# Kernel tuning notes

Measured on AMD Instinct MI355X. Metric: run time of the kernel, lower is better.

The kernel has to match this reference:

```python
import jax, jax.numpy as jnp
import numpy as np

EPS = 1e-5


def setup_inputs() -> dict:
    key = jax.random.key(0)
    ks = jax.random.split(key, 12)
    N, E, H, NIN = 50000, 800000, 128, 256  # nodes, edges, num_hidden, num_in
    D_IN = H + NIN  # 384, concat width
    src_na = jax.random.normal(ks[0], (N, H), dtype=jnp.float32)
    dst_na = jax.random.normal(ks[1], (N, H), dtype=jnp.float32)
    ea = jax.random.normal(ks[2], (E, H), dtype=jnp.float32)
    edge_idx = jax.random.randint(ks[3], (2, E), 0, N, dtype=jnp.int64)
    s = 0.05
    W11 = jax.random.normal(ks[4], (D_IN, H), dtype=jnp.float32) * s
    b11 = jnp.zeros((H,), dtype=jnp.float32)
    W12 = jax.random.normal(ks[5], (H, H), dtype=jnp.float32) * s
    b12 = jnp.zeros((H,), dtype=jnp.float32)
    W13 = jax.random.normal(ks[6], (H, H), dtype=jnp.float32) * s
    b13 = jnp.zeros((H,), dtype=jnp.float32)
    gamma = jnp.ones((H,), dtype=jnp.float32)
    beta = jnp.zeros((H,), dtype=jnp.float32)
    return {"src_na": src_na, "dst_na": dst_na, "ea": ea, "edge_idx": edge_idx,
            "W11": W11, "b11": b11, "W12": W12, "b12": b12,
            "W13": W13, "b13": b13, "gamma": gamma, "beta": beta}


def reference(src_na, dst_na, ea, edge_idx, W11, b11, W12, b12, W13, b13, gamma, beta):
    dst_idx = edge_idx[0]
    src_idx = edge_idx[1]
    # gather endpoint node features per edge, concat: [E, H + 2*H_node]
    h_EV = jnp.concatenate([src_na[src_idx], ea, dst_na[dst_idx]], axis=-1)
    gelu = lambda x: jax.nn.gelu(x, approximate=False)  # torch GELU is exact erf
    h = gelu(h_EV @ W11 + b11)
    h = gelu(h @ W12 + b12)
    h_message = h @ W13 + b13
    # dropout in eval mode = identity; BatchNorm1d with batch stats (training-style)
    x = ea + h_message
    mean = jnp.mean(x, axis=0)
    var = jnp.var(x, axis=0)  # biased, as BatchNorm uses for normalization
    ea_update = (x - mean) * jax.lax.rsqrt(var + EPS) * gamma + beta
    return ea_update
```

## Files before the change

kernel.cpp:

```cpp
#include <hip/hip_runtime.h>
#include <hip/hip_fp16.h>

#define HD 128
#define BM 128

typedef _Float16 f16x8 __attribute__((ext_vector_type(8)));
typedef float f32x4 __attribute__((ext_vector_type(4)));

#define W11H_OFF 0
#define W11L_OFF 49152
#define W12H_OFF 98304
#define W12L_OFF 114688
#define W13H_OFF 131072
#define W13L_OFF 147456

__device__ __forceinline__ float gelu_exact(float x) {
  return 0.5f * x * (1.0f + erff(x * 0.70710678118654752f));
}

__global__ __launch_bounds__(256) void repack_w(
    const float* __restrict__ W11, const float* __restrict__ W12,
    const float* __restrict__ W13, _Float16* __restrict__ wp)
{
  int t = blockIdx.x * 256 + threadIdx.x;
  const float* W; int local, hb, lb;
  if (t < 6144)      { W = W11; local = t;        hb = W11H_OFF; lb = W11L_OFF; }
  else if (t < 8192) { W = W12; local = t - 6144; hb = W12H_OFF; lb = W12L_OFF; }
  else               { W = W13; local = t - 8192; hb = W13H_OFF; lb = W13L_OFF; }
  int frag = local >> 6, lane = local & 63;
  int k0  = (frag >> 3) * 32 + ((lane >> 4) * 8);
  int col = (frag & 7) * 16 + (lane & 15);
  _Float16* Hp = wp + hb + (size_t)local * 8;
  _Float16* Lp = wp + lb + (size_t)local * 8;
#pragma unroll
  for (int i = 0; i < 8; ++i) {
    float w = W[(size_t)(k0 + i) * HD + col];
    _Float16 h = (_Float16)w;
    Hp[i] = h;
    Lp[i] = (_Float16)(w - (float)h);
  }
}

__global__ __launch_bounds__(256, 2) void fused_mlp(
    const float* __restrict__ src_na, const float* __restrict__ dst_na,
    const float* __restrict__ ea, const int* __restrict__ eidx,
    const float* __restrict__ b11, const float* __restrict__ b12,
    const float* __restrict__ b13, const _Float16* __restrict__ wp,
    float* __restrict__ stats, float* __restrict__ xout, int E)
{
  __shared__ unsigned int hsm[4 * 32 * HD];
  const int tid  = threadIdx.x;
  const int lane = tid & 63;
  const int wave = tid >> 6;
  const int l15  = lane & 15;
  const int lg   = lane >> 4;
  const int e0   = blockIdx.x * BM + wave * 32;
  unsigned int* myh = hsm + wave * 32 * HD;

  int erow[2], sidx[2], didx[2];
#pragma unroll
  for (int m = 0; m < 2; ++m) {
    int e = e0 + m * 16 + l15;
    e = e < E ? e : E - 1;
    erow[m] = e;
    didx[m] = eidx[e];
    sidx[m] = eidx[E + e];
  }

  const f32x4 vzero = {0.f, 0.f, 0.f, 0.f};
  f32x4 acc[2][8];
#pragma unroll
  for (int m = 0; m < 2; ++m)
#pragma unroll
    for (int f = 0; f < 8; ++f) acc[m][f] = vzero;

  const _Float16* w11h = wp + W11H_OFF;
  const _Float16* w11l = wp + W11L_OFF;
#pragma unroll 2
  for (int ks = 0; ks < 12; ++ks) {
    const int part = ks >> 2;
    const int kc = (ks & 3) * 32 + lg * 8;
    f16x8 ah[2], al[2];
#pragma unroll
    for (int m = 0; m < 2; ++m) {
      const float* rp;
      if (part == 0)      rp = src_na + (size_t)sidx[m] * HD;
      else if (part == 1) rp = ea + (size_t)erow[m] * HD;
      else                rp = dst_na + (size_t)didx[m] * HD;
      float4 v0 = *(const float4*)(rp + kc);
      float4 v1 = *(const float4*)(rp + kc + 4);
      float v[8] = {v0.x, v0.y, v0.z, v0.w, v1.x, v1.y, v1.z, v1.w};
#pragma unroll
      for (int i = 0; i < 8; ++i) {
        _Float16 hh = (_Float16)v[i];
        ah[m][i] = hh;
        al[m][i] = (_Float16)(v[i] - (float)hh);
      }
    }
    const _Float16* bhp = w11h + (size_t)(ks * 8) * 512 + lane * 8;
    const _Float16* blp = w11l + (size_t)(ks * 8) * 512 + lane * 8;
#pragma unroll
    for (int fc = 0; fc < 8; ++fc) {
      f16x8 bh = *(const f16x8*)(bhp + fc * 512);
      f16x8 bl = *(const f16x8*)(blp + fc * 512);
#pragma unroll
      for (int m = 0; m < 2; ++m) {
        acc[m][fc] = __builtin_amdgcn_mfma_f32_16x16x32_f16(ah[m], bh, acc[m][fc], 0, 0, 0);
        acc[m][fc] = __builtin_amdgcn_mfma_f32_16x16x32_f16(ah[m], bl, acc[m][fc], 0, 0, 0);
        acc[m][fc] = __builtin_amdgcn_mfma_f32_16x16x32_f16(al[m], bh, acc[m][fc], 0, 0, 0);
      }
    }
  }

  auto store_h = [&](const float* __restrict__ bias) {
#pragma unroll
    for (int fc = 0; fc < 8; ++fc) {
      int col = fc * 16 + l15;
      float b = bias[col];
#pragma unroll
      for (int m = 0; m < 2; ++m)
#pragma unroll
        for (int r = 0; r < 4; ++r) {
          int row = m * 16 + lg * 4 + r;
          float hv = gelu_exact(acc[m][fc][r] + b);
          _Float16 hh = (_Float16)hv;
          _Float16 hl = (_Float16)(hv - (float)hh);
          unsigned int u = ((unsigned int)__builtin_bit_cast(unsigned short, hh) << 16)
                         | (unsigned int)__builtin_bit_cast(unsigned short, hl);
          unsigned int off = (unsigned int)(row * HD + col) * 4u;
          off ^= ((unsigned int)(row & 7)) << 4;
          *(unsigned int*)((char*)myh + off) = u;
        }
    }
  };

  auto mlp_layer = [&](const _Float16* __restrict__ wh, const _Float16* __restrict__ wl) {
#pragma unroll
    for (int m = 0; m < 2; ++m)
#pragma unroll
      for (int f = 0; f < 8; ++f) acc[m][f] = vzero;
#pragma unroll
    for (int ks = 0; ks < 4; ++ks) {
      f16x8 ah[2], al[2];
#pragma unroll
      for (int m = 0; m < 2; ++m) {
        int row = m * 16 + l15;
        unsigned int base = (unsigned int)(row * HD + ks * 32 + lg * 8) * 4u;
        unsigned int sz = ((unsigned int)(row & 7)) << 4;
        uint4 q0 = *(const uint4*)((const char*)myh + (base ^ sz));
        uint4 q1 = *(const uint4*)((const char*)myh + ((base + 16) ^ sz));
        unsigned int uu[8] = {q0.x, q0.y, q0.z, q0.w, q1.x, q1.y, q1.z, q1.w};
#pragma unroll
        for (int i = 0; i < 8; ++i) {
          ah[m][i] = __builtin_bit_cast(_Float16, (unsigned short)(uu[i] >> 16));
          al[m][i] = __builtin_bit_cast(_Float16, (unsigned short)(uu[i] & 0xffffu));
        }
      }
      const _Float16* bhp = wh + (size_t)(ks * 8) * 512 + lane * 8;
      const _Float16* blp = wl + (size_t)(ks * 8) * 512 + lane * 8;
#pragma unroll
      for (int fc = 0; fc < 8; ++fc) {
        f16x8 bh = *(const f16x8*)(bhp + fc * 512);
        f16x8 bl = *(const f16x8*)(blp + fc * 512);
#pragma unroll
        for (int m = 0; m < 2; ++m) {
          acc[m][fc] = __builtin_amdgcn_mfma_f32_16x16x32_f16(ah[m], bh, acc[m][fc], 0, 0, 0);
          acc[m][fc] = __builtin_amdgcn_mfma_f32_16x16x32_f16(ah[m], bl, acc[m][fc], 0, 0, 0);
          acc[m][fc] = __builtin_amdgcn_mfma_f32_16x16x32_f16(al[m], bh, acc[m][fc], 0, 0, 0);
        }
      }
    }
  };

  store_h(b11);
  mlp_layer(wp + W12H_OFF, wp + W12L_OFF);
  store_h(b12);
  mlp_layer(wp + W13H_OFF, wp + W13L_OFF);

#pragma unroll
  for (int fc = 0; fc < 8; ++fc) {
    int col = fc * 16 + l15;
    float b = b13[col];
    float s = 0.f, sq = 0.f;
#pragma unroll
    for (int m = 0; m < 2; ++m)
#pragma unroll
      for (int r = 0; r < 4; ++r) {
        int row = m * 16 + lg * 4 + r;
        int e = e0 + row;
        bool valid = e < E;
        e = valid ? e : E - 1;
        float x = acc[m][fc][r] + b + ea[(size_t)e * HD + col];
        xout[(size_t)e * HD + col] = x;
        float xv = valid ? x : 0.f;
        s += xv; sq += xv * xv;
      }
    s  += __shfl_xor(s, 16);  s  += __shfl_xor(s, 32);
    sq += __shfl_xor(sq, 16); sq += __shfl_xor(sq, 32);
    if (lg == 0) {
      atomicAdd(&stats[col], s);
      atomicAdd(&stats[HD + col], sq);
    }
  }
}

__global__ void bn_finalize(float* __restrict__ stats, const float* __restrict__ gamma,
                            const float* __restrict__ beta, float invE)
{
  int c = threadIdx.x;
  if (c < HD) {
    float mean = stats[c] * invE;
    float var  = stats[HD + c] * invE - mean * mean;
    float sc   = gamma[c] * rsqrtf(var + 1e-5f);
    stats[2 * HD + c] = sc;
    stats[3 * HD + c] = beta[c] - mean * sc;
  }
}

__global__ __launch_bounds__(256) void bn_apply(float* __restrict__ x,
                                                const float* __restrict__ stats,
                                                long long n4)
{
  __shared__ float4 s_sc[32], s_sh[32];
  if (threadIdx.x < 32) {
    s_sc[threadIdx.x] = ((const float4*)(stats + 2 * HD))[threadIdx.x];
    s_sh[threadIdx.x] = ((const float4*)(stats + 3 * HD))[threadIdx.x];
  }
  __syncthreads();
  long long i = (long long)blockIdx.x * 256 + threadIdx.x;
  const long long stride = (long long)gridDim.x * 256;
  float4* __restrict__ x4 = (float4*)x;
  for (; i < n4; i += stride) {
    float4 v = x4[i];
    int c4 = (int)(i & 31);
    float4 a = s_sc[c4], b = s_sh[c4];
    v.x = v.x * a.x + b.x;
    v.y = v.y * a.y + b.y;
    v.z = v.z * a.z + b.z;
    v.w = v.w * a.w + b.w;
    x4[i] = v;
  }
}

extern "C" void kernel_launch(void* const* d_in, const int* in_sizes, int n_in,
                              void* d_out, int out_size, void* d_ws, size_t ws_size,
                              hipStream_t stream) {
  const float* src_na = (const float*)d_in[0];
  const float* dst_na = (const float*)d_in[1];
  const float* ea     = (const float*)d_in[2];
  const int*   eidx   = (const int*)d_in[3];
  const float* W11    = (const float*)d_in[4];
  const float* b11    = (const float*)d_in[5];
  const float* W12    = (const float*)d_in[6];
  const float* b12    = (const float*)d_in[7];
  const float* W13    = (const float*)d_in[8];
  const float* b13    = (const float*)d_in[9];
  const float* gamma  = (const float*)d_in[10];
  const float* beta   = (const float*)d_in[11];
  const int E = in_sizes[3] / 2;

  float*    stats = (float*)d_ws;
  _Float16* wp    = (_Float16*)((char*)d_ws + 4096);
  float*    xout  = (float*)d_out;

  hipMemsetAsync(d_ws, 0, 1024, stream);
  repack_w<<<40, 256, 0, stream>>>(W11, W12, W13, wp);
  fused_mlp<<<(E + BM - 1) / BM, 256, 0, stream>>>(src_na, dst_na, ea, eidx,
                                                   b11, b12, b13, wp, stats, xout, E);
  bn_finalize<<<1, 128, 0, stream>>>(stats, gamma, beta, 1.0f / (float)E);
  long long n4 = (long long)E * HD / 4;
  bn_apply<<<4096, 256, 0, stream>>>(xout, stats, n4);
}
```

Before: 1.616 ms.

## Batch gather loads per input part and shrink fused MLP blocks to two waves

After: 1.778 ms. +10.1%, slower.

```diff
diff --git a/kernel.cpp b/kernel.cpp
--- a/kernel.cpp
+++ b/kernel.cpp
@@ -2,7 +2,7 @@
 #include <hip/hip_fp16.h>
 
 #define HD 128
-#define BM 128
+#define BM 64
 
 typedef _Float16 f16x8 __attribute__((ext_vector_type(8)));
 typedef float f32x4 __attribute__((ext_vector_type(4)));
@@ -41,14 +41,14 @@
   }
 }
 
-__global__ __launch_bounds__(256, 2) void fused_mlp(
+__global__ __launch_bounds__(128, 2) void fused_mlp(
     const float* __restrict__ src_na, const float* __restrict__ dst_na,
     const float* __restrict__ ea, const int* __restrict__ eidx,
     const float* __restrict__ b11, const float* __restrict__ b12,
     const float* __restrict__ b13, const _Float16* __restrict__ wp,
     float* __restrict__ stats, float* __restrict__ xout, int E)
 {
-  __shared__ unsigned int hsm[4 * 32 * HD];
+  __shared__ unsigned int hsm[2 * 32 * HD];
   const int tid  = threadIdx.x;
   const int lane = tid & 63;
   const int wave = tid >> 6;
@@ -76,38 +76,50 @@
 
   const _Float16* w11h = wp + W11H_OFF;
   const _Float16* w11l = wp + W11L_OFF;
-#pragma unroll 2
-  for (int ks = 0; ks < 12; ++ks) {
-    const int part = ks >> 2;
-    const int kc = (ks & 3) * 32 + lg * 8;
-    f16x8 ah[2], al[2];
+#pragma unroll
+  for (int part = 0; part < 3; ++part) {
+    float4 vv[2][8];
 #pragma unroll
     for (int m = 0; m < 2; ++m) {
       const float* rp;
       if (part == 0)      rp = src_na + (size_t)sidx[m] * HD;
       else if (part == 1) rp = ea + (size_t)erow[m] * HD;
       else                rp = dst_na + (size_t)didx[m] * HD;
-      float4 v0 = *(const float4*)(rp + kc);
-      float4 v1 = *(const float4*)(rp + kc + 4);
-      float v[8] = {v0.x, v0.y, v0.z, v0.w, v1.x, v1.y, v1.z, v1.w};
-#pragma unroll
-      for (int i = 0; i < 8; ++i) {
-        _Float16 hh = (_Float16)v[i];
-        ah[m][i] = hh;
-        al[m][i] = (_Float16)(v[i] - (float)hh);
-      }
-    }
-    const _Float16* bhp = w11h + (size_t)(ks * 8) * 512 + lane * 8;
-    const _Float16* blp = w11l + (size_t)(ks * 8) * 512 + lane * 8;
-#pragma unroll
-    for (int fc = 0; fc < 8; ++fc) {
-      f16x8 bh = *(const f16x8*)(bhp + fc * 512);
-      f16x8 bl = *(const f16x8*)(blp + fc * 512);
-#pragma unroll
-      for (int m = 0; m < 2; ++m) {
-        acc[m][fc] = __builtin_amdgcn_mfma_f32_16x16x32_f16(ah[m], bh, acc[m][fc], 0, 0, 0);
-        acc[m][fc] = __builtin_amdgcn_mfma_f32_16x16x32_f16(ah[m], bl, acc[m][fc], 0, 0, 0);
-        acc[m][fc] = __builtin_amdgcn_mfma_f32_16x16x32_f16(al[m], bh, acc[m][fc], 0, 0, 0);
+#pragma unroll
+      for (int q = 0; q < 4; ++q) {
+        vv[m][2 * q]     = *(const float4*)(rp + q * 32 + lg * 8);
+        vv[m][2 * q + 1] = *(const float4*)(rp + q * 32 + lg * 8 + 4);
+      }
+    }
+    f16x8 ah[2][4], al[2][4];
+#pragma unroll
+    for (int m = 0; m < 2; ++m)
+#pragma unroll
+      for (int q = 0; q < 4; ++q) {
+        float v[8] = {vv[m][2*q].x, vv[m][2*q].y, vv[m][2*q].z, vv[m][2*q].w,
+                      vv[m][2*q+1].x, vv[m][2*q+1].y, vv[m][2*q+1].z, vv[m][2*q+1].w};
+#pragma unroll
+        for (int i = 0; i < 8; ++i) {
+          _Float16 hh = (_Float16)v[i];
+          ah[m][q][i] = hh;
+          al[m][q][i] = (_Float16)(v[i] - (float)hh);
+        }
+      }
+#pragma unroll
+    for (int q = 0; q < 4; ++q) {
+      const int ks = part * 4 + q;
+      const _Float16* bhp = w11h + (size_t)(ks * 8) * 512 + lane * 8;
+      const _Float16* blp = w11l + (size_t)(ks * 8) * 512 + lane * 8;
+#pragma unroll
+      for (int fc = 0; fc < 8; ++fc) {
+        f16x8 bh = *(const f16x8*)(bhp + fc * 512);
+        f16x8 bl = *(const f16x8*)(blp + fc * 512);
+#pragma unroll
+        for (int m = 0; m < 2; ++m) {
+          acc[m][fc] = __builtin_amdgcn_mfma_f32_16x16x32_f16(ah[m][q], bh, acc[m][fc], 0, 0, 0);
+          acc[m][fc] = __builtin_amdgcn_mfma_f32_16x16x32_f16(ah[m][q], bl, acc[m][fc], 0, 0, 0);
+          acc[m][fc] = __builtin_amdgcn_mfma_f32_16x16x32_f16(al[m][q], bh, acc[m][fc], 0, 0, 0);
+        }
       }
     }
   }
@@ -265,9 +277,9 @@
 
   hipMemsetAsync(d_ws, 0, 1024, stream);
   repack_w<<<40, 256, 0, stream>>>(W11, W12, W13, wp);
-  fused_mlp<<<(E + BM - 1) / BM, 256, 0, stream>>>(src_na, dst_na, ea, eidx,
+  fused_mlp<<<(E + BM - 1) / BM, 128, 0, stream>>>(src_na, dst_na, ea, eidx,
                                                    b11, b12, b13, wp, stats, xout, E);
   bn_finalize<<<1, 128, 0, stream>>>(stats, gamma, beta, 1.0f / (float)E);
   long long n4 = (long long)E * HD / 4;
-  bn_apply<<<4096, 256, 0, stream>>>(xout, stats, n4);
-}
+  bn_apply<<<8192, 256, 0, stream>>>(xout, stats, n4);
+}
```
